# Performance work log

Hardware: AMD Instinct MI355X
Metric: run time of the kernel (lower is better)

Reference implementation:

```python
import jax, jax.numpy as jnp
import numpy as np
import math

B_, L_, D_, N_ = 8, 2048, 1024, 64


def _ln(x, g, b):
    m = jnp.mean(x, axis=-1, keepdims=True)
    v = jnp.mean((x - m) ** 2, axis=-1, keepdims=True)
    return (x - m) / jnp.sqrt(v + 1e-5) * g + b


def _ssm_kernel(A, Bp, Cp, Dp, L):
    # diagonal SSM: lambda = exp(diag(A)); k[l] = C diag(lambda)^l B + D  -> shape (L,)
    a = jnp.diagonal(A)                                   # (N,)
    powers = jnp.exp(jnp.arange(L)[:, None] * a[None, :])  # (L, N) = lambda^l
    return powers @ (Bp[:, 0] * Cp[0]) + Dp[0]             # (L,)


def _causal_conv(h, k):
    # y[:, t, :] = sum_{j<=t} k[j] * h[:, t-j, :]  via zero-padded FFT (same math, O(L log L))
    L = h.shape[1]
    n = 2 * L
    Hf = jnp.fft.rfft(h, n=n, axis=1)
    Kf = jnp.fft.rfft(k, n=n)
    return jnp.fft.irfft(Hf * Kf[None, :, None], n=n, axis=1)[:, :L]


def _timestep_embedding(t, dim):
    half = dim // 2
    freqs = jnp.exp(jnp.arange(half) * (-math.log(10000.0) / (half - 1)))
    ang = t[:, None] * freqs[None, :]
    return jnp.concatenate([jnp.sin(ang), jnp.cos(ang)], axis=1)  # (B, dim)


def _conv1d(x, w, b):
    # x: (B, C, L), w: (O, I, 3) torch layout, padding=1
    y = jax.lax.conv_general_dilated(x, w, (1,), [(1, 1)],
                                     dimension_numbers=('NCH', 'OIH', 'NCH'))
    return y + b[None, :, None]


def setup_inputs():
    key = jax.random.key(0)
    ks = jax.random.split(key, 26)
    d = {}
    d['x'] = jax.random.normal(ks[0], (B_, L_, D_), jnp.float32)
    d['t'] = jax.random.uniform(ks[1], (B_,), jnp.float32) * 1000.0
    d['beta1'] = jax.random.uniform(ks[2], (1,), jnp.float32)
    d['beta2'] = jax.random.uniform(ks[3], (1,), jnp.float32)
    sc = 1.0 / math.sqrt(D_)
    d['Wi'] = jax.random.normal(ks[4], (D_, D_), jnp.float32) * sc
    d['bi'] = jnp.zeros((D_,), jnp.float32)
    d['Wo'] = jax.random.normal(ks[5], (D_, D_), jnp.float32) * sc
    d['bo'] = jnp.zeros((D_,), jnp.float32)
    d['w1'] = jax.random.normal(ks[6], (D_, D_, 3), jnp.float32) * 0.02
    d['bc1'] = jnp.zeros((D_,), jnp.float32)
    d['w2'] = jax.random.normal(ks[7], (D_, D_, 3), jnp.float32) * 0.02
    d['bc2'] = jnp.zeros((D_,), jnp.float32)
    d['g1'] = jnp.ones((D_,), jnp.float32)
    d['b1'] = jnp.zeros((D_,), jnp.float32)
    d['g2'] = jnp.ones((D_,), jnp.float32)
    d['b2'] = jnp.zeros((D_,), jnp.float32)
    # SSM params (std 0.001 on A keeps exp(l*a) bounded for l up to L)
    d['Af'] = jax.random.normal(ks[8], (N_, N_), jnp.float32) * 0.001
    d['Bf'] = jax.random.normal(ks[9], (N_, 1), jnp.float32) * 0.01
    d['Cf'] = jax.random.normal(ks[10], (1, N_), jnp.float32) * 0.01
    d['Df'] = jax.random.normal(ks[11], (1,), jnp.float32) * 0.01
    d['Ab'] = jax.random.normal(ks[12], (N_, N_), jnp.float32) * 0.001
    d['Bb'] = jax.random.normal(ks[13], (N_, 1), jnp.float32) * 0.01
    d['Cb'] = jax.random.normal(ks[14], (1, N_), jnp.float32) * 0.01
    d['Db'] = jax.random.normal(ks[15], (1,), jnp.float32) * 0.01
    return d


def reference(x, t, beta1, beta2, Wi, bi, Wo, bo, w1, bc1, w2, bc2,
              g1, b1, g2, b2, Af, Bf, Cf, Df, Ab, Bb, Cb, Db):
    Bsz, L, D = x.shape
    h = x @ Wi + bi
    h = _ln(h, g1, b1)
    # local conv branch
    hT = jnp.transpose(h, (0, 2, 1))                 # (B, D, L)
    co = jax.nn.silu(_conv1d(hT, w1, bc1))
    co = _conv1d(co, w2, bc2)
    conv_out = jnp.transpose(co, (0, 2, 1))          # (B, L, D)
    # bidirectional SSM global convolutions
    kf = _ssm_kernel(Af, Bf, Cf, Df, L)
    h_fwd = _causal_conv(h, kf)
    kb = _ssm_kernel(Ab, Bb, Cb, Db, L)
    h_bwd = jnp.flip(_causal_conv(jnp.flip(h, axis=1), kb), axis=1)
    # timestep-conditioned mixing
    noise_scale = jax.nn.sigmoid(_timestep_embedding(t, D))[:, None, :]  # (B,1,D)
    h = h_fwd * (beta1[0] * noise_scale) + h_bwd * (beta2[0] * noise_scale) + conv_out
    h = h @ Wo + bo
    h = _ln(h, g2, b2)
    return x + h
```

## Files before the change

### kernel.cpp

```cpp
#include <hip/hip_runtime.h>

#define Bq 8
#define Lq 2048
#define Dq 1024
#define LPq 2050

typedef unsigned short u16;
typedef __attribute__((ext_vector_type(8))) short bf16x8;
typedef __attribute__((ext_vector_type(4))) float f32x4;

__device__ __forceinline__ u16 f2bf(float f) {
  unsigned u = __float_as_uint(f);
  u += 0x7FFFu + ((u >> 16) & 1u);
  return (u16)(u >> 16);
}
__device__ __forceinline__ float bf2f(u16 s) {
  return __uint_as_float(((unsigned)s) << 16);
}
__device__ __forceinline__ void gld16(const u16* g, u16* l) {
  __builtin_amdgcn_global_load_lds((const __attribute__((address_space(1))) void*)g,
                                   (__attribute__((address_space(3))) void*)l, 16, 0, 0);
}


__global__ __launch_bounds__(256) void prep_small(
    const float* __restrict__ t,
    const float* __restrict__ Af, const float* __restrict__ Bf, const float* __restrict__ Cf, const float* __restrict__ Df,
    const float* __restrict__ Ab, const float* __restrict__ Bb, const float* __restrict__ Cb, const float* __restrict__ Db,
    float* __restrict__ kf, float* __restrict__ kb,
    float* __restrict__ ns,
    u16* __restrict__ hpad, u16* __restrict__ copad) {
  int tid = blockIdx.x * 256 + threadIdx.x;
  if (blockIdx.x < 8) {
    int l = tid;
    float sf = Df[0], sb = Db[0];
    for (int n = 0; n < 64; n++) {
      sf += __expf((float)l * Af[n * 64 + n]) * (Bf[n] * Cf[n]);
      sb += __expf((float)l * Ab[n * 64 + n]) * (Bb[n] * Cb[n]);
    }
    kf[l] = sf; kb[l] = sb;
  } else if (blockIdx.x < 40) {
    int i = tid - 2048;
    int b = i >> 10, d = i & 1023;
    float tb = t[b];
    float e;
    if (d < 512) {
      float f = __expf((float)d * (-logf(10000.f) / 511.f));
      e = sinf(tb * f);
    } else {
      float f = __expf((float)(d - 512) * (-logf(10000.f) / 511.f));
      e = cosf(tb * f);
    }
    ns[i] = 1.f / (1.f + __expf(-e));
  } else {
    int i = tid - 10240;
    if (i < 32768) {
      int d = i & 1023;
      int j = i >> 10;
      int arr = j & 1, r = (j >> 1) & 1, b = j >> 2;
      size_t off = (size_t)b * LPq * Dq + (r ? (size_t)(LPq - 1) * Dq : 0) + d;
      if (arr == 0) hpad[off] = 0;
      else          copad[off] = 0;
    }
  }
}

__global__ __launch_bounds__(256) void mega_prep(
    const float* __restrict__ x, u16* __restrict__ xb,
    const float* __restrict__ Wi, u16* __restrict__ wit,
    const float* __restrict__ Wo, u16* __restrict__ wot,
    const float* __restrict__ w1, u16* __restrict__ w1t,
    const float* __restrict__ w2, u16* __restrict__ w2t,
    const float* __restrict__ kf, const float* __restrict__ kb,
    const float* __restrict__ be1, const float* __restrict__ be2,
    u16* __restrict__ Tm) {
  int bid = blockIdx.x, tid = threadIdx.x;
  if (bid < 8192) {
    size_t i = ((size_t)bid * 256 + tid) * 8;
    float4 a = *(const float4*)(x + i);
    float4 b = *(const float4*)(x + i + 4);
    u16 o[8] = {f2bf(a.x), f2bf(a.y), f2bf(a.z), f2bf(a.w),
                f2bf(b.x), f2bf(b.y), f2bf(b.z), f2bf(b.w)};
    *(bf16x8*)(xb + i) = *(const bf16x8*)o;
  } else if (bid < 8704) {
    __shared__ float tile[64][65];
    const float* W = (bid < 8448) ? Wi : Wo;
    u16* Wt = (bid < 8448) ? wit : wot;
    int b2 = (bid < 8448) ? bid - 8192 : bid - 8448;
    int bx = b2 & 15, by = b2 >> 4;
    int tx = tid & 63, tw = tid >> 6;
    for (int r = tw; r < 64; r += 4)
      tile[r][tx] = W[(size_t)(by * 64 + r) * 1024 + bx * 64 + tx];
    __syncthreads();
    for (int r = tw; r < 64; r += 4)
      Wt[(size_t)(bx * 64 + r) * 1024 + by * 64 + tx] = f2bf(tile[tx][r]);
  } else if (bid < 14848) {
    const float* w = (bid < 11776) ? w1 : w2;
    u16* Wt = (bid < 11776) ? w1t : w2t;
    int vb = (bid < 11776) ? bid - 8704 : bid - 11776;
    int base = (vb * 256 + tid) * 4;
    int o = base / 3072, rem = base % 3072;
    int dt = rem >> 10, i0 = rem & 1023;
    const float* src = w + (size_t)o * 3072 + dt;
    ushort4 v;
    v.x = f2bf(src[(i0 + 0) * 3]);
    v.y = f2bf(src[(i0 + 1) * 3]);
    v.z = f2bf(src[(i0 + 2) * 3]);
    v.w = f2bf(src[(i0 + 3) * 3]);
    *(ushort4*)(Wt + base) = v;
  } else {
    int idx = (bid - 14848) * 256 + tid;
    int tr = idx >> 9, j0 = (idx & 511) * 4;
    float b1v = be1[0], b2v = be2[0];
    ushort4 v;
#pragma unroll
    for (int q = 0; q < 4; q++) {
      int j = j0 + q;
      float vv = 0.f;
      if (tr >= j) vv += b1v * kf[tr - j];
      if (j >= tr) vv += b2v * kb[j - tr];
      ((u16*)&v)[q] = f2bf(vv);
    }
    *(ushort4*)(Tm + (size_t)tr * 2048 + j0) = v;
  }
}

__global__ __launch_bounds__(256) void trans_h(const u16* __restrict__ hpad, u16* __restrict__ ht) {
  __shared__ u16 tile[64][66];
  int b = blockIdx.z;
  int lt = blockIdx.x * 64, dt = blockIdx.y * 64;
  int tx = threadIdx.x & 15, ty = threadIdx.x >> 4;
  const u16* src = hpad + (size_t)b * LPq * Dq + (size_t)(lt + 1 + ty) * Dq + dt + tx * 4;
#pragma unroll
  for (int i = 0; i < 4; i++) {
    int r = ty + i * 16;
    ushort4 v = *(const ushort4*)(src + (size_t)i * 16 * Dq);
    tile[tx * 4 + 0][r] = v.x;
    tile[tx * 4 + 1][r] = v.y;
    tile[tx * 4 + 2][r] = v.z;
    tile[tx * 4 + 3][r] = v.w;
  }
  __syncthreads();
#pragma unroll
  for (int i = 0; i < 4; i++) {
    int d = ty + i * 16;
    ushort4 v;
    v.x = tile[d][tx * 4 + 0];
    v.y = tile[d][tx * 4 + 1];
    v.z = tile[d][tx * 4 + 2];
    v.w = tile[d][tx * 4 + 3];
    *(ushort4*)(ht + ((size_t)b * Dq + dt + d) * Lq + lt + tx * 4) = v;
  }
}


__global__ __launch_bounds__(256) void ln1_k(const u16* __restrict__ h0, u16* __restrict__ hpad,
                                             const float* __restrict__ g, const float* __restrict__ be) {
  int w = threadIdx.x >> 6, lane = threadIdx.x & 63;
  int r = blockIdx.x * 4 + w;
  int d0 = lane * 16;
  const u16* hp = h0 + (size_t)r * 1024 + d0;
  bf16x8 va = *(const bf16x8*)hp;
  bf16x8 vb = *(const bf16x8*)(hp + 8);
  float v[16];
#pragma unroll
  for (int i = 0; i < 8; i++) { v[i] = bf2f((u16)va[i]); v[8 + i] = bf2f((u16)vb[i]); }
  float s = 0.f, q = 0.f;
#pragma unroll
  for (int i = 0; i < 16; i++) { s += v[i]; q += v[i] * v[i]; }
#pragma unroll
  for (int o = 32; o > 0; o >>= 1) { s += __shfl_xor(s, o); q += __shfl_xor(q, o); }
  float mean = s * (1.f / 1024.f);
  float rstd = rsqrtf(q * (1.f / 1024.f) - mean * mean + 1e-5f);
  const float4* g4 = (const float4*)(g + d0);
  const float4* b4 = (const float4*)(be + d0);
  u16 o16[16];
#pragma unroll
  for (int i = 0; i < 4; i++) {
    float4 gv = g4[i], bv = b4[i];
    o16[i * 4 + 0] = f2bf((v[i * 4 + 0] - mean) * rstd * gv.x + bv.x);
    o16[i * 4 + 1] = f2bf((v[i * 4 + 1] - mean) * rstd * gv.y + bv.y);
    o16[i * 4 + 2] = f2bf((v[i * 4 + 2] - mean) * rstd * gv.z + bv.z);
    o16[i * 4 + 3] = f2bf((v[i * 4 + 3] - mean) * rstd * gv.w + bv.w);
  }
  int b_ = r >> 11, l = r & 2047;
  u16* dst = hpad + ((size_t)b_ * LPq + l + 1) * Dq + d0;
  *(bf16x8*)dst = *(const bf16x8*)o16;
  *(bf16x8*)(dst + 8) = *(const bf16x8*)(o16 + 8);
}

__global__ __launch_bounds__(256) void ln2_k(const u16* __restrict__ hp, const float* __restrict__ x,
                                             const float* __restrict__ g, const float* __restrict__ be,
                                             float* __restrict__ out) {
  int w = threadIdx.x >> 6, lane = threadIdx.x & 63;
  size_t r = (size_t)blockIdx.x * 4 + w;
  int d0 = lane * 16;
  size_t base = r * 1024 + d0;
  const u16* h = hp + base;
  bf16x8 va = *(const bf16x8*)h;
  bf16x8 vb = *(const bf16x8*)(h + 8);
  float v[16];
#pragma unroll
  for (int i = 0; i < 8; i++) { v[i] = bf2f((u16)va[i]); v[8 + i] = bf2f((u16)vb[i]); }
  float s = 0.f, q = 0.f;
#pragma unroll
  for (int i = 0; i < 16; i++) { s += v[i]; q += v[i] * v[i]; }
#pragma unroll
  for (int o = 32; o > 0; o >>= 1) { s += __shfl_xor(s, o); q += __shfl_xor(q, o); }
  float mean = s * (1.f / 1024.f);
  float rstd = rsqrtf(q * (1.f / 1024.f) - mean * mean + 1e-5f);
  const float4* g4 = (const float4*)(g + d0);
  const float4* b4 = (const float4*)(be + d0);
  const float4* x4 = (const float4*)(x + base);
  float4* o4 = (float4*)(out + base);
#pragma unroll
  for (int i = 0; i < 4; i++) {
    float4 gv = g4[i], bv = b4[i], xv = x4[i];
    float4 o;
    o.x = xv.x + (v[i * 4 + 0] - mean) * rstd * gv.x + bv.x;
    o.y = xv.y + (v[i * 4 + 1] - mean) * rstd * gv.y + bv.y;
    o.z = xv.z + (v[i * 4 + 2] - mean) * rstd * gv.z + bv.z;
    o.w = xv.w + (v[i * 4 + 3] - mean) * rstd * gv.w + bv.w;
    o4[i] = o;
  }
}

__device__ __forceinline__ void gemm_core(const u16* __restrict__ Ab, int lda,
                                          const u16* __restrict__ Bb, int ldb,
                                          int NS, u16* lds,
                                          f32x4 (&acc)[8][4]) {
  const int t = threadIdx.x;
  const int lane = t & 63, w = t >> 6;
  const int g = w >> 2, j = w & 3;
  int aoff[4], boff[4];
#pragma unroll
  for (int q = 0; q < 4; q++) {
    int c = t + q * 512;
    int row = c >> 3;
    int slot = (c & 7) ^ (row & 7);
    aoff[q] = row * lda + slot * 8;
    boff[q] = row * ldb + slot * 8;
  }
  const int frow = lane & 15, f = lane >> 4;
  int aadr[8], badr[4];
#pragma unroll
  for (int mf = 0; mf < 8; mf++) {
    int row = g * 128 + mf * 16 + frow;
    aadr[mf] = row * 64 + ((f ^ (row & 7)) << 3);
  }
#pragma unroll
  for (int nf = 0; nf < 4; nf++) {
    int row = j * 64 + nf * 16 + frow;
    badr[nf] = 16384 + row * 64 + ((f ^ (row & 7)) << 3);
  }

#define STAGE_A(s_) { const u16* g_ = Ab + (s_) * 64; u16* l_ = lds + ((s_) & 1) * 32768; \
    gld16(g_ + aoff[0], l_ + t * 8);            gld16(g_ + aoff[1], l_ + (t + 512) * 8); \
    gld16(g_ + aoff[2], l_ + (t + 1024) * 8);   gld16(g_ + aoff[3], l_ + (t + 1536) * 8); }
#define STAGE_B(s_) { const u16* g_ = Bb + (s_) * 64; u16* l_ = lds + ((s_) & 1) * 32768 + 16384; \
    gld16(g_ + boff[0], l_ + t * 8);            gld16(g_ + boff[1], l_ + (t + 512) * 8); \
    gld16(g_ + boff[2], l_ + (t + 1024) * 8);   gld16(g_ + boff[3], l_ + (t + 1536) * 8); }

  STAGE_A(0); STAGE_B(0);

  for (int s = 0; s < NS; s++) {
    const u16* sl = lds + (s & 1) * 32768;
    asm volatile("s_waitcnt vmcnt(0)" ::: "memory");
    asm volatile("s_barrier" ::: "memory");
    if (s + 1 < NS) STAGE_A(s + 1);
    bf16x8 bq[4], af[4];
#pragma unroll
    for (int nf = 0; nf < 4; nf++) bq[nf] = *(const bf16x8*)(sl + badr[nf]);
#pragma unroll
    for (int mf = 0; mf < 4; mf++) af[mf] = *(const bf16x8*)(sl + aadr[mf]);
    __builtin_amdgcn_s_setprio(1);
#pragma unroll
    for (int mf = 0; mf < 4; mf++)
#pragma unroll
      for (int nf = 0; nf < 4; nf++)
        acc[mf][nf] = __builtin_amdgcn_mfma_f32_16x16x32_bf16(af[mf], bq[nf], acc[mf][nf], 0, 0, 0);
    __builtin_amdgcn_s_setprio(0);
    if (s + 1 < NS) STAGE_B(s + 1);
#pragma unroll
    for (int mf = 0; mf < 4; mf++) af[mf] = *(const bf16x8*)(sl + aadr[4 + mf]);
    __builtin_amdgcn_s_setprio(1);
#pragma unroll
    for (int mf = 0; mf < 4; mf++)
#pragma unroll
      for (int nf = 0; nf < 4; nf++)
        acc[4 + mf][nf] = __builtin_amdgcn_mfma_f32_16x16x32_bf16(af[mf], bq[nf], acc[4 + mf][nf], 0, 0, 0);
    __builtin_amdgcn_s_setprio(0);
#pragma unroll
    for (int nf = 0; nf < 4; nf++) bq[nf] = *(const bf16x8*)(sl + (badr[nf] ^ 32));
#pragma unroll
    for (int mf = 0; mf < 4; mf++) af[mf] = *(const bf16x8*)(sl + (aadr[mf] ^ 32));
    __builtin_amdgcn_s_setprio(1);
#pragma unroll
    for (int mf = 0; mf < 4; mf++)
#pragma unroll
      for (int nf = 0; nf < 4; nf++)
        acc[mf][nf] = __builtin_amdgcn_mfma_f32_16x16x32_bf16(af[mf], bq[nf], acc[mf][nf], 0, 0, 0);
    __builtin_amdgcn_s_setprio(0);
#pragma unroll
    for (int mf = 0; mf < 4; mf++) af[mf] = *(const bf16x8*)(sl + (aadr[4 + mf] ^ 32));
    __builtin_amdgcn_s_setprio(1);
#pragma unroll
    for (int mf = 0; mf < 4; mf++)
#pragma unroll
      for (int nf = 0; nf < 4; nf++)
        acc[4 + mf][nf] = __builtin_amdgcn_mfma_f32_16x16x32_bf16(af[mf], bq[nf], acc[4 + mf][nf], 0, 0, 0);
    __builtin_amdgcn_s_setprio(0);
  }
#undef STAGE_A
#undef STAGE_B
}

template <int MODE>
__global__ __launch_bounds__(512, 2) void gemm8(
    const u16* __restrict__ A, int lda, long abstr,
    const u16* __restrict__ Bw, int ldb,
    u16* __restrict__ Out, long obstr,
    const float* __restrict__ bias, int K, int nbm) {
  __shared__ __align__(16) u16 lds[65536];
  int mb = blockIdx.x % nbm, nb = blockIdx.x / nbm;
  int m0 = mb * 256, n0 = nb * 256;
  int batch = m0 >> 11, r0 = m0 & 2047;
  const u16* Ab = A + (size_t)batch * abstr + (size_t)r0 * lda;
  const u16* Bb = Bw + (size_t)n0 * ldb;
  f32x4 acc[8][4] = {};
  gemm_core(Ab, lda, Bb, ldb, K >> 6, lds, acc);
  int lane = threadIdx.x & 63, w = threadIdx.x >> 6;
  int g = w >> 2, j = w & 3;
  int frow = lane & 15;
  u16* ob = Out + (size_t)batch * obstr;
#pragma unroll
  for (int mf = 0; mf < 8; mf++) {
    int row = r0 + g * 128 + mf * 16 + ((lane >> 4) << 2);
#pragma unroll
    for (int nf = 0; nf < 4; nf++) {
      int col = n0 + j * 64 + nf * 16 + frow;
      float bv = bias[col];
      size_t base = (size_t)row * 1024 + col;
      f32x4 a = acc[mf][nf];
#pragma unroll
      for (int i = 0; i < 4; i++) {
        float v = a[i] + bv;
        if (MODE == 1) v = v / (1.f + __expf(-v));
        if (MODE == 2) v += bf2f(ob[base + (size_t)i * 1024]);
        ob[base + (size_t)i * 1024] = f2bf(v);
      }
    }
  }
}

__global__ __launch_bounds__(512, 2) void mix8(
    const u16* __restrict__ hpad, const u16* __restrict__ w1t,
    u16* __restrict__ co, const float* __restrict__ bc1,
    const u16* __restrict__ Tm, const u16* __restrict__ Ht,
    const float* __restrict__ ns, u16* __restrict__ hmix) {
  __shared__ __align__(16) u16 lds[65536];
  const long PSTR = (long)LPq * 1024;
  int id = blockIdx.x;
  int lane = threadIdx.x & 63, w = threadIdx.x >> 6;
  int g = w >> 2, j = w & 3;
  int frow = lane & 15;
  if (id < 256) {
    int mb = id & 63, nb = id >> 6;
    int m0 = mb * 256, n0 = nb * 256;
    int batch = m0 >> 11, r0 = m0 & 2047;
    const u16* Ab = hpad + (size_t)batch * PSTR + (size_t)r0 * 1024;
    const u16* Bb = w1t + (size_t)n0 * 3072;
    f32x4 acc[8][4] = {};
    gemm_core(Ab, 1024, Bb, 3072, 48, lds, acc);
    u16* ob = co + (size_t)batch * PSTR;
#pragma unroll
    for (int mf = 0; mf < 8; mf++) {
      int row = r0 + g * 128 + mf * 16 + ((lane >> 4) << 2);
#pragma unroll
      for (int nf = 0; nf < 4; nf++) {
        int col = n0 + j * 64 + nf * 16 + frow;
        float bv = bc1[col];
        size_t base = (size_t)row * 1024 + col;
        f32x4 a = acc[mf][nf];
#pragma unroll
        for (int i = 0; i < 4; i++) {
          float v = a[i] + bv;
          v = v / (1.f + __expf(-v));
          ob[base + (size_t)i * 1024] = f2bf(v);
        }
      }
    }
  } else {
    int r = id - 256;
    int mb = r & 7, nb = r >> 3;
    int m0 = mb * 256, n0 = nb * 256;
    const u16* Ab = Tm + (size_t)m0 * 2048;
    const u16* Bb = Ht + (size_t)n0 * 2048;
    f32x4 acc[8][4] = {};
    gemm_core(Ab, 2048, Bb, 2048, 32, lds, acc);
#pragma unroll
    for (int mf = 0; mf < 8; mf++) {
      int row = m0 + g * 128 + mf * 16 + ((lane >> 4) << 2);
#pragma unroll
      for (int nf = 0; nf < 4; nf++) {
        int col = n0 + j * 64 + nf * 16 + frow;
        int b = col >> 10, d = col & 1023;
        float cv = ns[col];
        u16* op = hmix + ((size_t)b * Lq + row) * 1024 + d;
        f32x4 a = acc[mf][nf];
#pragma unroll
        for (int i = 0; i < 4; i++)
          op[(size_t)i * 1024] = f2bf(a[i] * cv);
      }
    }
  }
}


extern "C" void kernel_launch(void* const* d_in, const int* in_sizes, int n_in,
                              void* d_out, int out_size, void* d_ws, size_t ws_size,
                              hipStream_t stream) {
  const float* x   = (const float*)d_in[0];
  const float* tt  = (const float*)d_in[1];
  const float* be1 = (const float*)d_in[2];
  const float* be2 = (const float*)d_in[3];
  const float* Wi  = (const float*)d_in[4];
  const float* bi  = (const float*)d_in[5];
  const float* Wo  = (const float*)d_in[6];
  const float* bo  = (const float*)d_in[7];
  const float* w1  = (const float*)d_in[8];
  const float* bc1 = (const float*)d_in[9];
  const float* w2  = (const float*)d_in[10];
  const float* bc2 = (const float*)d_in[11];
  const float* g1  = (const float*)d_in[12];
  const float* b1  = (const float*)d_in[13];
  const float* g2  = (const float*)d_in[14];
  const float* b2  = (const float*)d_in[15];
  const float* Af  = (const float*)d_in[16];
  const float* Bf  = (const float*)d_in[17];
  const float* Cf  = (const float*)d_in[18];
  const float* Df  = (const float*)d_in[19];
  const float* Ab  = (const float*)d_in[20];
  const float* Bb  = (const float*)d_in[21];
  const float* Cb  = (const float*)d_in[22];
  const float* Db  = (const float*)d_in[23];

  char* p = (char*)d_ws;
  constexpr size_t SZ_h0   = (size_t)16384 * 1024 * 2;
  constexpr size_t SZ_hpad = (size_t)Bq * LPq * Dq * 2;
  constexpr size_t SZ_ht   = (size_t)Bq * Dq * Lq * 2;
  constexpr size_t SZ_hmix = (size_t)16384 * 1024 * 2;
  constexpr size_t SZ_T    = (size_t)2048 * 2048 * 2;
  constexpr size_t SZ_wt   = (size_t)1024 * 1024 * 2;
  constexpr size_t SZ_w3t  = (size_t)1024 * 3072 * 2;

  size_t off = 0;
  u16* h0    = (u16*)(p + off); off += SZ_h0;
  u16* hpad  = (u16*)(p + off); off += SZ_hpad;
  u16* ht    = (u16*)(p + off); off += SZ_ht;
  u16* copad = (u16*)(p + off); off += SZ_hpad;
  u16* hmixF = (u16*)(p + off); off += SZ_hmix;
  u16* Tmat  = (u16*)(p + off); off += SZ_T;
  u16* wit   = (u16*)(p + off); off += SZ_wt;
  u16* wot   = (u16*)(p + off); off += SZ_wt;
  u16* w1t   = (u16*)(p + off); off += SZ_w3t;
  u16* w2t   = (u16*)(p + off); off += SZ_w3t;
  float* kf  = (float*)(p + off); off += 8192;
  float* kb  = (float*)(p + off); off += 8192;
  float* nsb = (float*)(p + off); off += 32768;
  u16* xb    = hmixF;

  const long BSTR = (long)2048 * 1024;
  const long PSTR = (long)LPq * 1024;

  prep_small<<<dim3(168), dim3(256), 0, stream>>>(tt, Af, Bf, Cf, Df,
                                                  Ab, Bb, Cb, Db, kf, kb, nsb, hpad, copad);
  mega_prep<<<dim3(18944), dim3(256), 0, stream>>>(x, xb, Wi, wit, Wo, wot,
                                                   w1, w1t, w2, w2t, kf, kb, be1, be2, Tmat);

  gemm8<0><<<dim3(256), dim3(512), 0, stream>>>(xb, 1024, BSTR, wit, 1024, h0, BSTR, bi, 1024, 64);
  ln1_k<<<dim3(4096), dim3(256), 0, stream>>>(h0, hpad, g1, b1);
  trans_h<<<dim3(32, 16, 8), dim3(256), 0, stream>>>(hpad, ht);
  mix8<<<dim3(512), dim3(512), 0, stream>>>(hpad, w1t, copad + 1024, bc1,
                                            Tmat, ht, nsb, hmixF);
  gemm8<2><<<dim3(256), dim3(512), 0, stream>>>(copad, 1024, PSTR, w2t, 3072, hmixF, BSTR, bc2, 3072, 64);
  gemm8<0><<<dim3(256), dim3(512), 0, stream>>>(hmixF, 1024, BSTR, wot, 1024, h0, BSTR, bo, 1024, 64);
  ln2_k<<<dim3(4096), dim3(256), 0, stream>>>(h0, x, g2, b2, (float*)d_out);
}
```

Baseline: 407.3 us.

## Load GEMM B-operand fragments directly from global into registers, bypassing LDS

```diff
diff --git a/kernel.cpp b/kernel.cpp
--- a/kernel.cpp
+++ b/kernel.cpp
@@ -231,46 +231,46 @@
                                           f32x4 (&acc)[8][4]) {
   const int t = threadIdx.x;
   const int lane = t & 63, w = t >> 6;
-  const int g = w >> 2, j = w & 3;
-  int aoff[4], boff[4];
+  const int g = w >> 2;
+  const int j = __builtin_amdgcn_readfirstlane(w & 3);
+  int aoff[4];
 #pragma unroll
   for (int q = 0; q < 4; q++) {
     int c = t + q * 512;
     int row = c >> 3;
     int slot = (c & 7) ^ (row & 7);
     aoff[q] = row * lda + slot * 8;
-    boff[q] = row * ldb + slot * 8;
   }
   const int frow = lane & 15, f = lane >> 4;
-  int aadr[8], badr[4];
+  int aadr[8];
 #pragma unroll
   for (int mf = 0; mf < 8; mf++) {
     int row = g * 128 + mf * 16 + frow;
     aadr[mf] = row * 64 + ((f ^ (row & 7)) << 3);
   }
-#pragma unroll
-  for (int nf = 0; nf < 4; nf++) {
-    int row = j * 64 + nf * 16 + frow;
-    badr[nf] = 16384 + row * 64 + ((f ^ (row & 7)) << 3);
-  }
-
-#define STAGE_A(s_) { const u16* g_ = Ab + (s_) * 64; u16* l_ = lds + ((s_) & 1) * 32768; \
-    gld16(g_ + aoff[0], l_ + t * 8);            gld16(g_ + aoff[1], l_ + (t + 512) * 8); \
-    gld16(g_ + aoff[2], l_ + (t + 1024) * 8);   gld16(g_ + aoff[3], l_ + (t + 1536) * 8); }
-#define STAGE_B(s_) { const u16* g_ = Bb + (s_) * 64; u16* l_ = lds + ((s_) & 1) * 32768 + 16384; \
-    gld16(g_ + boff[0], l_ + t * 8);            gld16(g_ + boff[1], l_ + (t + 512) * 8); \
-    gld16(g_ + boff[2], l_ + (t + 1024) * 8);   gld16(g_ + boff[3], l_ + (t + 1536) * 8); }
-
-  STAGE_A(0); STAGE_B(0);
+  const u16* bn[4];
+#pragma unroll
+  for (int nf = 0; nf < 4; nf++)
+    bn[nf] = Bb + (size_t)(j * 64 + nf * 16 + frow) * ldb + f * 8;
+  bf16x8 bq0[4], bq1[4];
+
+#define STAGE_A(s_) { const u16* g_ = Ab + (s_) * 64; u16* l_ = lds + ((s_) & 1) * 16384; \
+    _Pragma("unroll") for (int q = 0; q < 4; q++) gld16(g_ + aoff[q], l_ + (t + q * 512) * 8); }
+#define LOAD_B0(s_) { _Pragma("unroll") for (int nf = 0; nf < 4; nf++) \
+    bq0[nf] = *(const bf16x8*)(bn[nf] + (s_) * 64); }
+#define LOAD_B1(s_) { _Pragma("unroll") for (int nf = 0; nf < 4; nf++) \
+    bq1[nf] = *(const bf16x8*)(bn[nf] + (s_) * 64 + 32); }
+
+  STAGE_A(0);
+  LOAD_B0(0);
+  LOAD_B1(0);
 
   for (int s = 0; s < NS; s++) {
-    const u16* sl = lds + (s & 1) * 32768;
+    const u16* sl = lds + (s & 1) * 16384;
     asm volatile("s_waitcnt vmcnt(0)" ::: "memory");
     asm volatile("s_barrier" ::: "memory");
     if (s + 1 < NS) STAGE_A(s + 1);
-    bf16x8 bq[4], af[4];
-#pragma unroll
-    for (int nf = 0; nf < 4; nf++) bq[nf] = *(const bf16x8*)(sl + badr[nf]);
+    bf16x8 af[4];
 #pragma unroll
     for (int mf = 0; mf < 4; mf++) af[mf] = *(const bf16x8*)(sl + aadr[mf]);
     __builtin_amdgcn_s_setprio(1);
@@ -278,9 +278,8 @@
     for (int mf = 0; mf < 4; mf++)
 #pragma unroll
       for (int nf = 0; nf < 4; nf++)
-        acc[mf][nf] = __builtin_amdgcn_mfma_f32_16x16x32_bf16(af[mf], bq[nf], acc[mf][nf], 0, 0, 0);
+        acc[mf][nf] = __builtin_amdgcn_mfma_f32_16x16x32_bf16(af[mf], bq0[nf], acc[mf][nf], 0, 0, 0);
     __builtin_amdgcn_s_setprio(0);
-    if (s + 1 < NS) STAGE_B(s + 1);
 #pragma unroll
     for (int mf = 0; mf < 4; mf++) af[mf] = *(const bf16x8*)(sl + aadr[4 + mf]);
     __builtin_amdgcn_s_setprio(1);
@@ -288,10 +287,10 @@
     for (int mf = 0; mf < 4; mf++)
 #pragma unroll
       for (int nf = 0; nf < 4; nf++)
-        acc[4 + mf][nf] = __builtin_amdgcn_mfma_f32_16x16x32_bf16(af[mf], bq[nf], acc[4 + mf][nf], 0, 0, 0);
+        acc[4 + mf][nf] = __builtin_amdgcn_mfma_f32_16x16x32_bf16(af[mf], bq0[nf], acc[4 + mf][nf], 0, 0, 0);
     __builtin_amdgcn_s_setprio(0);
-#pragma unroll
-    for (int nf = 0; nf < 4; nf++) bq[nf] = *(const bf16x8*)(sl + (badr[nf] ^ 32));
+    __builtin_amdgcn_sched_barrier(0);
+    if (s + 1 < NS) LOAD_B0(s + 1);
 #pragma unroll
     for (int mf = 0; mf < 4; mf++) af[mf] = *(const bf16x8*)(sl + (aadr[mf] ^ 32));
     __builtin_amdgcn_s_setprio(1);
@@ -299,7 +298,7 @@
     for (int mf = 0; mf < 4; mf++)
 #pragma unroll
       for (int nf = 0; nf < 4; nf++)
-        acc[mf][nf] = __builtin_amdgcn_mfma_f32_16x16x32_bf16(af[mf], bq[nf], acc[mf][nf], 0, 0, 0);
+        acc[mf][nf] = __builtin_amdgcn_mfma_f32_16x16x32_bf16(af[mf], bq1[nf], acc[mf][nf], 0, 0, 0);
     __builtin_amdgcn_s_setprio(0);
 #pragma unroll
     for (int mf = 0; mf < 4; mf++) af[mf] = *(const bf16x8*)(sl + (aadr[4 + mf] ^ 32));
@@ -308,11 +307,14 @@
     for (int mf = 0; mf < 4; mf++)
 #pragma unroll
       for (int nf = 0; nf < 4; nf++)
-        acc[4 + mf][nf] = __builtin_amdgcn_mfma_f32_16x16x32_bf16(af[mf], bq[nf], acc[4 + mf][nf], 0, 0, 0);
+        acc[4 + mf][nf] = __builtin_amdgcn_mfma_f32_16x16x32_bf16(af[mf], bq1[nf], acc[4 + mf][nf], 0, 0, 0);
     __builtin_amdgcn_s_setprio(0);
+    __builtin_amdgcn_sched_barrier(0);
+    if (s + 1 < NS) LOAD_B1(s + 1);
   }
 #undef STAGE_A
-#undef STAGE_B
+#undef LOAD_B0
+#undef LOAD_B1
 }
 
 template <int MODE>
@@ -321,7 +323,7 @@
     const u16* __restrict__ Bw, int ldb,
     u16* __restrict__ Out, long obstr,
     const float* __restrict__ bias, int K, int nbm) {
-  __shared__ __align__(16) u16 lds[65536];
+  __shared__ __align__(16) u16 lds[32768];
   int mb = blockIdx.x % nbm, nb = blockIdx.x / nbm;
   int m0 = mb * 256, n0 = nb * 256;
   int batch = m0 >> 11, r0 = m0 & 2047;
@@ -358,7 +360,7 @@
     u16* __restrict__ co, const float* __restrict__ bc1,
     const u16* __restrict__ Tm, const u16* __restrict__ Ht,
     const float* __restrict__ ns, u16* __restrict__ hmix) {
-  __shared__ __align__(16) u16 lds[65536];
+  __shared__ __align__(16) u16 lds[32768];
   const long PSTR = (long)LPq * 1024;
   int id = blockIdx.x;
   int lane = threadIdx.x & 63, w = threadIdx.x >> 6;
```

Result: slower. 636.9 us (+56.4%).
